# Performance work log

Measured on AMD Instinct MI355X. Metric: run time of the kernel, lower is better.

The kernel has to match this reference:

```python
import jax, jax.numpy as jnp
import numpy as np

B, N, DEG = 8, 4096, 16
E = N * DEG            # edges per graph
IN, HID, C, OUT = 128, 512, 2, 10
EPS = 1e-15


def setup_inputs() -> dict:
    key = jax.random.key(0)
    ks = jax.random.split(key, 16)
    # within-graph random edges, then offset each graph by b*N
    src = jax.random.randint(ks[0], (B, E), 0, N)
    dst = jax.random.randint(ks[1], (B, E), 0, N)
    off = (jnp.arange(B) * N)[:, None]
    edge_index = jnp.stack([(src + off).reshape(-1), (dst + off).reshape(-1)], axis=0).astype(jnp.int64)
    batch = jnp.repeat(jnp.arange(B), N).astype(jnp.int64)
    x = jax.random.normal(ks[2], (B * N, IN), dtype=jnp.float32)
    edge_weight = jax.random.uniform(ks[3], (B * E,), dtype=jnp.float32)
    g = lambda k, s: (0.02 * jax.random.normal(k, s, dtype=jnp.float32))
    return {
        "x": x, "edge_index": edge_index, "batch": batch, "edge_weight": edge_weight,
        "W_rel1": g(ks[4], (IN, HID)), "b_rel1": jnp.zeros((HID,), jnp.float32),
        "W_root1": g(ks[5], (IN, HID)),
        "W_pool": g(ks[6], (HID, C)), "b_pool": jnp.zeros((C,), jnp.float32),
        "W_rel3": g(ks[7], (HID, HID)), "b_rel3": jnp.zeros((HID,), jnp.float32),
        "W_root3": g(ks[8], (HID, HID)),
        "W_lin1": g(ks[9], (HID, HID)), "b_lin1": jnp.zeros((HID,), jnp.float32),
        "W_lin2": g(ks[10], (HID, OUT)), "b_lin2": jnp.zeros((OUT,), jnp.float32),
    }


def reference(x, edge_index, batch, edge_weight,
              W_rel1, b_rel1, W_root1, W_pool, b_pool,
              W_rel3, b_rel3, W_root3, W_lin1, b_lin1, W_lin2, b_lin2):
    src, dst = edge_index[0], edge_index[1]
    # GraphConv (aggr='add'): out = lin_rel(sum_j w_ji x_j) + lin_root(x)
    agg = jax.ops.segment_sum(x[src] * edge_weight[:, None], dst, num_segments=B * N)
    h = jax.nn.relu(agg @ W_rel1 + b_rel1 + x @ W_root1)          # [BN, HID]
    s_logits = h @ W_pool + b_pool                                 # [BN, C]

    # dense batched tensors (equal-size graphs)
    hd = h.reshape(B, N, HID)
    s = jax.nn.softmax(s_logits.reshape(B, N, C), axis=-1)
    b_idx = batch[src]
    r = src - b_idx * N
    c = dst - b_idx * N
    adj = jnp.zeros((B, N, N), jnp.float32).at[b_idx, r, c].add(edge_weight)

    # dense mincut pooling
    out = jnp.einsum('bnc,bnf->bcf', s, hd)                        # [B, C, HID]
    sA = jnp.einsum('bnc,bnm->bcm', s, adj)
    out_adj = jnp.einsum('bcm,bmk->bck', sA, s)                    # [B, C, C]
    mincut_num = jnp.einsum('bcc->b', out_adj)
    d = adj.sum(-1)                                                # [B, N]
    mincut_den = jnp.einsum('bnc,bn,bnc->b', s, d, s)
    mc_loss = jnp.mean(-(mincut_num / mincut_den))
    ss = jnp.einsum('bnc,bnk->bck', s, s)
    ss_n = ss / jnp.linalg.norm(ss, axis=(1, 2), keepdims=True)
    i_s = jnp.eye(C, dtype=jnp.float32) / jnp.sqrt(jnp.float32(C))
    o_loss = jnp.mean(jnp.linalg.norm(ss_n - i_s[None], axis=(1, 2)))
    # zero diagonal + symmetric degree normalization
    out_adj = out_adj * (1.0 - jnp.eye(C, dtype=jnp.float32))[None]
    d2 = jnp.sqrt(out_adj.sum(-1)) + EPS                           # [B, C]
    out_adj = out_adj / d2[:, :, None] / d2[:, None, :]

    # conv3 on pooled graph: edges (row->col) of dense adj => agg = A^T x
    agg3 = jnp.einsum('bij,bif->bjf', out_adj, out)
    x3 = agg3 @ W_rel3 + b_rel3 + out @ W_root3                    # [B, C, HID]
    xm = x3.mean(axis=1)                                           # [B, HID]
    h2 = jax.nn.relu(xm @ W_lin1 + b_lin1)
    logits = h2 @ W_lin2 + b_lin2
    return (jax.nn.log_softmax(logits, axis=-1), mc_loss, o_loss, s_logits, out_adj)
```

## Files before the change

### kernel.cpp

```cpp
#include <hip/hip_runtime.h>
#include <hip/hip_bf16.h>

#define BB 8
#define NN 4096
#define EE 65536
#define BE (BB*EE)
#define BN (BB*NN)
#define INF 128
#define HID 512
#define CC 2
#define OUTC 10
#define ELLCAP 64

typedef __bf16 bf16x8_t __attribute__((ext_vector_type(8)));
typedef float  f32x4_t  __attribute__((ext_vector_type(4)));

__device__ __forceinline__ ushort f2bf(float f) {
  union { float f; unsigned u; } v; v.f = f;
  unsigned r = v.u + 0x7FFFu + ((v.u >> 16) & 1u);
  return (ushort)(r >> 16);
}
__device__ __forceinline__ float bf2f(ushort s) {
  union { unsigned u; float f; } v; v.u = ((unsigned)s) << 16;
  return v.f;
}

__global__ __launch_bounds__(256) void front(
    const int* __restrict__ src, const int* __restrict__ dst,
    const float* __restrict__ ew, const float* __restrict__ x,
    const float* __restrict__ Wrel, const float* __restrict__ Wroot,
    int* __restrict__ deg, int2* __restrict__ ell,
    ushort* __restrict__ Ab, ushort* __restrict__ Bb) {
  int blk = blockIdx.x;
  int tid = threadIdx.x;
  if (blk < 4096) {
    int g = (blk & 7) * 131072 + (blk >> 3) * 256 + tid;
    float4 v = *(const float4*)&x[(size_t)g * 4];
    int m = g >> 5;
    int kin = (g & 31) * 4;
    ushort4 o;
    o.x = f2bf(v.x); o.y = f2bf(v.y); o.z = f2bf(v.z); o.w = f2bf(v.w);
    *(ushort4*)&Ab[(size_t)m * 256 + 128 + kin] = o;
  } else if (blk < 6144) {
    int bl = blk - 4096;
    int e = (bl & 7) * EE + (bl >> 3) * 256 + tid;
    int d = dst[e];
    int p = atomicAdd(&deg[d], 1);
    if (p < ELLCAP) {
      int2 v; v.x = src[e]; v.y = __float_as_int(ew[e]);
      ell[(size_t)d * ELLCAP + p] = v;
    }
  } else {
    int g = (blk - 6144) * 256 + tid;
    int n = g & 511, k = g >> 9;
    float w = (k < 128) ? Wrel[k * 512 + n] : Wroot[(k - 128) * 512 + n];
    Bb[n * 256 + k] = f2bf(w);
  }
}

__global__ __launch_bounds__(256) void gather_ell(
    const int* __restrict__ deg, const int2* __restrict__ ell,
    ushort* __restrict__ Ab) {
  int blk = blockIdx.x;
  int n = (blk & 7) * NN + (blk >> 3) * 4 + (threadIdx.x >> 6);
  int lane = threadIdx.x & 63;
  int l4 = lane >> 4;
  int fl = lane & 15;
  int d = deg[n]; if (d > ELLCAP) d = ELLCAP;
  const int2* ep = ell + (size_t)n * ELLCAP;

  float a[8] = {0, 0, 0, 0, 0, 0, 0, 0};
  int j = 0;
  for (; j + 7 < d; j += 8) {
    int2 v0 = ep[j + l4];
    int2 v1 = ep[j + 4 + l4];
    uint4 u0 = *(const uint4*)&Ab[(size_t)v0.x * 256 + 128 + fl * 8];
    uint4 u1 = *(const uint4*)&Ab[(size_t)v1.x * 256 + 128 + fl * 8];
    float w0 = __int_as_float(v0.y);
    float w1 = __int_as_float(v1.y);
    const ushort* s0 = (const ushort*)&u0;
    const ushort* s1 = (const ushort*)&u1;
#pragma unroll
    for (int q = 0; q < 8; ++q)
      a[q] += w0 * bf2f(s0[q]) + w1 * bf2f(s1[q]);
  }
  for (; j + 3 < d; j += 4) {
    int2 v0 = ep[j + l4];
    uint4 u0 = *(const uint4*)&Ab[(size_t)v0.x * 256 + 128 + fl * 8];
    float w0 = __int_as_float(v0.y);
    const ushort* s0 = (const ushort*)&u0;
#pragma unroll
    for (int q = 0; q < 8; ++q)
      a[q] += w0 * bf2f(s0[q]);
  }
  {
    int idx = j + l4;
    if (idx < d) {
      int2 v0 = ep[idx];
      uint4 u0 = *(const uint4*)&Ab[(size_t)v0.x * 256 + 128 + fl * 8];
      float w0 = __int_as_float(v0.y);
      const ushort* s0 = (const ushort*)&u0;
#pragma unroll
      for (int q = 0; q < 8; ++q)
        a[q] += w0 * bf2f(s0[q]);
    }
  }
#pragma unroll
  for (int q = 0; q < 8; ++q) {
    a[q] += __shfl_xor(a[q], 16, 64);
    a[q] += __shfl_xor(a[q], 32, 64);
  }
  if (l4 == 0) {
    ushort o[8];
#pragma unroll
    for (int q = 0; q < 8; ++q) o[q] = f2bf(a[q]);
    *(uint4*)&Ab[(size_t)n * 256 + fl * 8] = *(const uint4*)o;
  }
}

__global__ __launch_bounds__(256) void gemm_pool(
    const ushort* __restrict__ Ab, const ushort* __restrict__ Bb,
    const float* __restrict__ brel, const float* __restrict__ Wp,
    const float* __restrict__ bp, float* __restrict__ s,
    float* __restrict__ slog, float* __restrict__ outpart,
    float* __restrict__ ssacc) {
  __shared__ ushort As[64 * 256];
  __shared__ ushort Bs[64 * 256];
  __shared__ ushort hS[64 * 512];
  __shared__ float ssr[4][3];
  int tid = threadIdx.x;
  int blk = blockIdx.x;
  int b = blk & 7;
  int chunk = blk >> 3;
  int m0 = b * NN + chunk * 64;
  int obik = b * 64 + chunk;

#pragma unroll
  for (int i = 0; i < 8; ++i) {
    int g = tid + i * 256;
    int r = g >> 5, c = g & 31;
    int cs = c ^ (r & 31);
    *(uint4*)&As[(r * 32 + cs) * 8] = *(const uint4*)&Ab[(size_t)(m0 + r) * 256 + c * 8];
  }

  int wave = tid >> 6, lane = tid & 63;
  int wm = wave * 16;
  int l16 = lane & 15, quad = lane >> 4;
  int arow = wm + l16;

  for (int cc = 0; cc < 8; ++cc) {
    int n0 = cc * 64;
#pragma unroll
    for (int i = 0; i < 8; ++i) {
      int g = tid + i * 256;
      int r = g >> 5, c = g & 31;
      int cs = c ^ (r & 31);
      *(uint4*)&Bs[(r * 32 + cs) * 8] = *(const uint4*)&Bb[(size_t)(n0 + r) * 256 + c * 8];
    }
    __syncthreads();

    f32x4_t acc[4];
#pragma unroll
    for (int ct = 0; ct < 4; ++ct) acc[ct] = (f32x4_t){0.f, 0.f, 0.f, 0.f};
#pragma unroll
    for (int kc = 0; kc < 8; ++kc) {
      int cl = kc * 4 + quad;
      bf16x8_t af = *(const bf16x8_t*)&As[(arow * 32 + (cl ^ (arow & 31))) * 8];
#pragma unroll
      for (int ct = 0; ct < 4; ++ct) {
        int brow = ct * 16 + l16;
        bf16x8_t bf = *(const bf16x8_t*)&Bs[(brow * 32 + (cl ^ (brow & 31))) * 8];
        acc[ct] = __builtin_amdgcn_mfma_f32_16x16x32_bf16(af, bf, acc[ct], 0, 0, 0);
      }
    }
#pragma unroll
    for (int ct = 0; ct < 4; ++ct) {
      int col = n0 + ct * 16 + l16;
      float bias = brel[col];
      int rowb = wm + quad * 4;
#pragma unroll
      for (int r = 0; r < 4; ++r)
        hS[(rowb + r) * 512 + col] = f2bf(fmaxf(acc[ct][r] + bias, 0.f));
    }
    __syncthreads();
  }

  int f0 = lane * 8;
  float wp0[8], wp1[8];
#pragma unroll
  for (int j = 0; j < 8; ++j) {
    wp0[j] = Wp[(f0 + j) * 2];
    wp1[j] = Wp[(f0 + j) * 2 + 1];
  }
  float bp0 = bp[0], bp1 = bp[1];
  float o0[8] = {0, 0, 0, 0, 0, 0, 0, 0};
  float o1[8] = {0, 0, 0, 0, 0, 0, 0, 0};
  float sa = 0.f, sb = 0.f, sc2 = 0.f;

  for (int i = 0; i < 16; ++i) {
    int nl = wm + i;
    int n = m0 + nl;
    bf16x8_t hv = *(const bf16x8_t*)&hS[(size_t)nl * 512 + f0];
    const ushort* hp = (const ushort*)&hv;
    float h[8];
    float a0 = 0.f, a1 = 0.f;
#pragma unroll
    for (int j = 0; j < 8; ++j) {
      h[j] = bf2f(hp[j]);
      a0 += h[j] * wp0[j];
      a1 += h[j] * wp1[j];
    }
#pragma unroll
    for (int off = 32; off; off >>= 1) {
      a0 += __shfl_down(a0, off, 64);
      a1 += __shfl_down(a1, off, 64);
    }
    float s0 = 0.f, s1 = 0.f;
    if (lane == 0) {
      float l0 = a0 + bp0, l1 = a1 + bp1;
      slog[n * 2] = l0;
      slog[n * 2 + 1] = l1;
      float m = fmaxf(l0, l1);
      float e0 = expf(l0 - m), e1 = expf(l1 - m);
      float inv = 1.f / (e0 + e1);
      s0 = e0 * inv; s1 = e1 * inv;
      s[n * 2] = s0;
      s[n * 2 + 1] = s1;
      sa += s0 * s0; sb += s0 * s1; sc2 += s1 * s1;
    }
    s0 = __shfl(s0, 0, 64);
    s1 = __shfl(s1, 0, 64);
#pragma unroll
    for (int j = 0; j < 8; ++j) {
      o0[j] += s0 * h[j];
      o1[j] += s1 * h[j];
    }
  }

  float* red = (float*)As;
#pragma unroll
  for (int j = 0; j < 8; ++j) {
    red[wave * 1024 + f0 + j] = o0[j];
    red[wave * 1024 + 512 + f0 + j] = o1[j];
  }
  if (lane == 0) { ssr[wave][0] = sa; ssr[wave][1] = sb; ssr[wave][2] = sc2; }
  __syncthreads();
#pragma unroll
  for (int q = 0; q < 4; ++q) {
    int idx = tid + q * 256;
    float v = red[idx] + red[1024 + idx] + red[2048 + idx] + red[3072 + idx];
    outpart[(size_t)obik * 1024 + idx] = v;
  }
  if (tid < 3) {
    float v = ssr[0][tid] + ssr[1][tid] + ssr[2][tid] + ssr[3][tid];
    atomicAdd(&ssacc[b * 4 + tid], v);
  }
}

__global__ __launch_bounds__(256) void edge_pass2(
    const int* __restrict__ src, const int* __restrict__ dst,
    const float* __restrict__ ew, const float* __restrict__ s,
    float* __restrict__ oadj, float* __restrict__ mden) {
  int b = blockIdx.x & 7;
  int sub = blockIdx.x >> 3;
  int base = b * EE + sub * 1024;
  float p00 = 0, p01 = 0, p10 = 0, p11 = 0, md = 0;
  for (int i = threadIdx.x; i < 1024; i += 256) {
    int e = base + i;
    int r = src[e], c = dst[e];
    float w = ew[e];
    float s0r = s[r * 2], s1r = s[r * 2 + 1];
    float s0c = s[c * 2], s1c = s[c * 2 + 1];
    p00 += w * s0r * s0c; p01 += w * s0r * s1c;
    p10 += w * s1r * s0c; p11 += w * s1r * s1c;
    md  += w * (s0r * s0r + s1r * s1r);
  }
#pragma unroll
  for (int off = 32; off; off >>= 1) {
    p00 += __shfl_down(p00, off, 64);
    p01 += __shfl_down(p01, off, 64);
    p10 += __shfl_down(p10, off, 64);
    p11 += __shfl_down(p11, off, 64);
    md  += __shfl_down(md,  off, 64);
  }
  __shared__ float red[4][5];
  int wave = threadIdx.x >> 6, lane = threadIdx.x & 63;
  if (lane == 0) {
    red[wave][0] = p00; red[wave][1] = p01;
    red[wave][2] = p10; red[wave][3] = p11;
    red[wave][4] = md;
  }
  __syncthreads();
  if (threadIdx.x < 4) {
    float v = red[0][threadIdx.x] + red[1][threadIdx.x] +
              red[2][threadIdx.x] + red[3][threadIdx.x];
    atomicAdd(&oadj[b * 4 + threadIdx.x], v);
  } else if (threadIdx.x == 4) {
    float v = red[0][4] + red[1][4] + red[2][4] + red[3][4];
    atomicAdd(&mden[b], v);
  }
}

__global__ __launch_bounds__(256) void finalize_a(
    const float* __restrict__ outpart, const float* __restrict__ oadj,
    const float* __restrict__ ssacc, const float* __restrict__ mden,
    float* __restrict__ uv, float* __restrict__ lossp,
    float* __restrict__ dout) {
  __shared__ float sc[2];
  __shared__ float r0[256], r1[256];
  int b = blockIdx.x >> 3, fc = blockIdx.x & 7;
  int t = threadIdx.x;
  if (t == 0) {
    float r00 = oadj[b * 4 + 0], r01 = oadj[b * 4 + 1];
    float r10 = oadj[b * 4 + 2], r11 = oadj[b * 4 + 3];
    float d20 = sqrtf(r01) + 1e-15f;
    float d21 = sqrtf(r10) + 1e-15f;
    float oa01 = r01 / (d20 * d21);
    float oa10 = r10 / (d21 * d20);
    sc[0] = oa01; sc[1] = oa10;
    if (fc == 0) {
      lossp[b * 2 + 0] = -((r00 + r11) / mden[b]) / (float)BB;
      float a = ssacc[b * 4 + 0], bb = ssacc[b * 4 + 1], c = ssacc[b * 4 + 2];
      float nrm = sqrtf(a * a + 2.f * bb * bb + c * c);
      float q = 0.70710678118654752f;
      float da = a / nrm - q, db = bb / nrm, dc = c / nrm - q;
      lossp[b * 2 + 1] = sqrtf(da * da + 2.f * db * db + dc * dc) / (float)BB;
      dout[65618 + b * 4 + 0] = 0.f;
      dout[65618 + b * 4 + 1] = oa01;
      dout[65618 + b * 4 + 2] = oa10;
      dout[65618 + b * 4 + 3] = 0.f;
    }
  }
  __syncthreads();
  int f = fc * 64 + (t & 63);
  int ic = t >> 6;
  float o0s = 0.f, o1s = 0.f;
  for (int i = ic * 16; i < ic * 16 + 16; ++i) {
    o0s += outpart[(size_t)(b * 64 + i) * 1024 + f];
    o1s += outpart[(size_t)(b * 64 + i) * 1024 + 512 + f];
  }
  r0[ic * 64 + (t & 63)] = o0s;
  r1[ic * 64 + (t & 63)] = o1s;
  __syncthreads();
  if (ic == 0) {
    int fl = t & 63;
    float a0 = r0[fl] + r0[64 + fl] + r0[128 + fl] + r0[192 + fl];
    float a1 = r1[fl] + r1[64 + fl] + r1[128 + fl] + r1[192 + fl];
    uv[b * HID + f] = sc[1] * a1 + sc[0] * a0;
    uv[BB * HID + b * HID + f] = a0 + a1;
  }
}

__global__ __launch_bounds__(256) void conv3_part(
    const float* __restrict__ uv, const float* __restrict__ Wrel3,
    const float* __restrict__ Wroot3, float* __restrict__ xmacc) {
  __shared__ float us[8][32], vs[8][32];
  __shared__ float red[4][64][8];
  int blk = blockIdx.x;
  int fc = blk & 7, kc = blk >> 3;
  int t = threadIdx.x;
  {
    int b = t >> 5, k = t & 31;
    us[b][k] = uv[b * HID + kc * 32 + k];
    vs[b][k] = uv[BB * HID + b * HID + kc * 32 + k];
  }
  __syncthreads();
  int f = fc * 64 + (t & 63);
  int ks = t >> 6;
  float acc[8] = {0, 0, 0, 0, 0, 0, 0, 0};
#pragma unroll
  for (int j = 0; j < 8; ++j) {
    int kl = ks * 8 + j;
    int k = kc * 32 + kl;
    float wr = Wrel3[k * HID + f];
    float wo = Wroot3[k * HID + f];
#pragma unroll
    for (int b = 0; b < 8; ++b)
      acc[b] += us[b][kl] * wr + vs[b][kl] * wo;
  }
#pragma unroll
  for (int b = 0; b < 8; ++b) red[ks][t & 63][b] = acc[b];
  __syncthreads();
  if (ks == 0) {
    int fl = t & 63;
#pragma unroll
    for (int b = 0; b < 8; ++b) {
      float v = red[0][fl][b] + red[1][fl][b] + red[2][fl][b] + red[3][fl][b];
      atomicAdd(&xmacc[b * HID + f], v);
    }
  }
}

__global__ __launch_bounds__(256) void lin1_part(
    const float* __restrict__ xmacc, const float* __restrict__ brel3,
    const float* __restrict__ Wlin1, float* __restrict__ h2acc) {
  __shared__ float xs[8][32];
  __shared__ float red[4][64][8];
  int blk = blockIdx.x;
  int fc = blk & 7, kc = blk >> 3;
  int t = threadIdx.x;
  {
    int b = t >> 5, k = t & 31;
    xs[b][k] = 0.5f * xmacc[b * HID + kc * 32 + k] + brel3[kc * 32 + k];
  }
  __syncthreads();
  int f = fc * 64 + (t & 63);
  int ks = t >> 6;
  float acc[8] = {0, 0, 0, 0, 0, 0, 0, 0};
#pragma unroll
  for (int j = 0; j < 8; ++j) {
    int kl = ks * 8 + j;
    int k = kc * 32 + kl;
    float w = Wlin1[k * HID + f];
#pragma unroll
    for (int b = 0; b < 8; ++b)
      acc[b] += xs[b][kl] * w;
  }
#pragma unroll
  for (int b = 0; b < 8; ++b) red[ks][t & 63][b] = acc[b];
  __syncthreads();
  if (ks == 0) {
    int fl = t & 63;
#pragma unroll
    for (int b = 0; b < 8; ++b) {
      float v = red[0][fl][b] + red[1][fl][b] + red[2][fl][b] + red[3][fl][b];
      atomicAdd(&h2acc[b * HID + f], v);
    }
  }
}

__global__ __launch_bounds__(256) void head(
    const float* __restrict__ h2acc, const float* __restrict__ blin1,
    const float* __restrict__ Wlin2, const float* __restrict__ blin2,
    const float* __restrict__ lossp, float* __restrict__ dout) {
  __shared__ float hs[HID];
  __shared__ float lg[16];
  __shared__ float lse;
  int b = blockIdx.x, t = threadIdx.x;
  if (b == 0 && t == 255) {
    float l0 = 0.f, l1 = 0.f;
#pragma unroll
    for (int i = 0; i < BB; ++i) { l0 += lossp[i * 2]; l1 += lossp[i * 2 + 1]; }
    dout[80] = l0;
    dout[81] = l1;
  }
  for (int i = t; i < HID; i += 256)
    hs[i] = fmaxf(h2acc[b * HID + i] + blin1[i], 0.f);
  __syncthreads();
  int wave = t >> 6, lane = t & 63;
  for (int o = wave; o < OUTC; o += 4) {
    float acc = 0.f;
    for (int k = lane; k < HID; k += 64)
      acc += hs[k] * Wlin2[k * OUTC + o];
#pragma unroll
    for (int off = 32; off; off >>= 1) acc += __shfl_down(acc, off, 64);
    if (lane == 0) lg[o] = acc + blin2[o];
  }
  __syncthreads();
  if (t == 0) {
    float m = lg[0];
    for (int o = 1; o < OUTC; ++o) m = fmaxf(m, lg[o]);
    float se = 0.f;
    for (int o = 0; o < OUTC; ++o) se += expf(lg[o] - m);
    lse = m + logf(se);
  }
  __syncthreads();
  if (t < OUTC) dout[b * OUTC + t] = lg[t] - lse;
}

extern "C" void kernel_launch(void* const* d_in, const int* in_sizes, int n_in,
                              void* d_out, int out_size, void* d_ws, size_t ws_size,
                              hipStream_t stream) {
  const float* x      = (const float*)d_in[0];
  const int*   ei     = (const int*)d_in[1];
  const float* ew     = (const float*)d_in[3];
  const float* Wrel1  = (const float*)d_in[4];
  const float* brel1  = (const float*)d_in[5];
  const float* Wroot1 = (const float*)d_in[6];
  const float* Wpool  = (const float*)d_in[7];
  const float* bpool  = (const float*)d_in[8];
  const float* Wrel3  = (const float*)d_in[9];
  const float* brel3  = (const float*)d_in[10];
  const float* Wroot3 = (const float*)d_in[11];
  const float* Wlin1  = (const float*)d_in[12];
  const float* blin1  = (const float*)d_in[13];
  const float* Wlin2  = (const float*)d_in[14];
  const float* blin2  = (const float*)d_in[15];
  float* out = (float*)d_out;
  float* ws  = (float*)d_ws;

  float* oadj  = ws + 40960;
  float* ssacc = oadj + 32;
  float* mden  = ssacc + 32;
  int*   deg   = (int*)(mden + 8);
  float* xmacc = ws + 73800;
  float* h2acc = xmacc + 4096;
  float* lossp = ws + 81992;
  ushort* Ab   = (ushort*)(ws + 106568);
  ushort* Bb   = (ushort*)(ws + 4300872);
  float* outpart = ws + 12763208;
  float* s     = ws + 16000000;
  int2*  ell   = (int2*)(ws + 4366408);
  float* uv    = (float*)deg;

  const int* src = ei;
  const int* dst = ei + BE;

  hipMemsetAsync(ws + 40960, 0, (size_t)41032 * sizeof(float), stream);

  front      <<<6656, 256, 0, stream>>>(src, dst, ew, x, Wrel1, Wroot1,
                                        deg, ell, Ab, Bb);
  gather_ell <<<BN / 4, 256, 0, stream>>>(deg, ell, Ab);
  gemm_pool  <<<512, 256, 0, stream>>>(Ab, Bb, brel1, Wpool, bpool,
                                       s, out + 82, outpart, ssacc);
  edge_pass2 <<<BB * 64, 256, 0, stream>>>(src, dst, ew, s, oadj, mden);
  finalize_a <<<64, 256, 0, stream>>>(outpart, oadj, ssacc, mden, uv, lossp, out);
  conv3_part <<<128, 256, 0, stream>>>(uv, Wrel3, Wroot3, xmacc);
  lin1_part  <<<128, 256, 0, stream>>>(xmacc, brel3, Wlin1, h2acc);
  head       <<<BB, 256, 0, stream>>>(h2acc, blin1, Wlin2, blin2, lossp, out);
}
```

Baseline: 209.7 us.

## Recompute conv1 GEMM in gemm_pool instead of staging h in LDS

Drops the 64 KB LDS buffer that held the bf16 hidden tile. The pool logits are now accumulated straight from the MFMA outputs, and the whole GEMM is run a second time to build the softmax-weighted feature sums, which are reduced into a small LDS array with atomics. This cuts LDS use per block so more blocks can be resident. In exchange it doubles the MFMA work and the B-matrix loads.

```diff
diff --git a/kernel.cpp b/kernel.cpp
--- a/kernel.cpp
+++ b/kernel.cpp
@@ -126,8 +126,11 @@
     float* __restrict__ ssacc) {
   __shared__ ushort As[64 * 256];
   __shared__ ushort Bs[64 * 256];
-  __shared__ ushort hS[64 * 512];
-  __shared__ float ssr[4][3];
+  __shared__ float wpS[1024];
+  __shared__ float brS[512];
+  __shared__ float2 ssv[64];
+  __shared__ float ssrw[16][3];
+  __shared__ float oacc[1024];
   int tid = threadIdx.x;
   int blk = blockIdx.x;
   int b = blk & 7;
@@ -142,11 +145,17 @@
     int cs = c ^ (r & 31);
     *(uint4*)&As[(r * 32 + cs) * 8] = *(const uint4*)&Ab[(size_t)(m0 + r) * 256 + c * 8];
   }
+  *(float4*)&wpS[tid * 4] = *(const float4*)&Wp[tid * 4];
+  if (tid < 128) *(float4*)&brS[tid * 4] = *(const float4*)&brel[tid * 4];
+  *(float4*)&oacc[tid * 4] = (float4){0.f, 0.f, 0.f, 0.f};
 
   int wave = tid >> 6, lane = tid & 63;
   int wm = wave * 16;
   int l16 = lane & 15, quad = lane >> 4;
   int arow = wm + l16;
+  float bp0 = bp[0], bp1 = bp[1];
+
+  float la0[4] = {0, 0, 0, 0}, la1[4] = {0, 0, 0, 0};
 
   for (int cc = 0; cc < 8; ++cc) {
     int n0 = cc * 64;
@@ -176,83 +185,105 @@
 #pragma unroll
     for (int ct = 0; ct < 4; ++ct) {
       int col = n0 + ct * 16 + l16;
-      float bias = brel[col];
-      int rowb = wm + quad * 4;
-#pragma unroll
-      for (int r = 0; r < 4; ++r)
-        hS[(rowb + r) * 512 + col] = f2bf(fmaxf(acc[ct][r] + bias, 0.f));
+      float bias = brS[col];
+      float w0 = wpS[col * 2], w1 = wpS[col * 2 + 1];
+#pragma unroll
+      for (int r = 0; r < 4; ++r) {
+        float h = fmaxf(acc[ct][r] + bias, 0.f);
+        la0[r] += h * w0;
+        la1[r] += h * w1;
+      }
     }
     __syncthreads();
   }
 
-  int f0 = lane * 8;
-  float wp0[8], wp1[8];
-#pragma unroll
-  for (int j = 0; j < 8; ++j) {
-    wp0[j] = Wp[(f0 + j) * 2];
-    wp1[j] = Wp[(f0 + j) * 2 + 1];
-  }
-  float bp0 = bp[0], bp1 = bp[1];
-  float o0[8] = {0, 0, 0, 0, 0, 0, 0, 0};
-  float o1[8] = {0, 0, 0, 0, 0, 0, 0, 0};
-  float sa = 0.f, sb = 0.f, sc2 = 0.f;
-
-  for (int i = 0; i < 16; ++i) {
-    int nl = wm + i;
-    int n = m0 + nl;
-    bf16x8_t hv = *(const bf16x8_t*)&hS[(size_t)nl * 512 + f0];
-    const ushort* hp = (const ushort*)&hv;
-    float h[8];
-    float a0 = 0.f, a1 = 0.f;
-#pragma unroll
-    for (int j = 0; j < 8; ++j) {
-      h[j] = bf2f(hp[j]);
-      a0 += h[j] * wp0[j];
-      a1 += h[j] * wp1[j];
-    }
-#pragma unroll
-    for (int off = 32; off; off >>= 1) {
-      a0 += __shfl_down(a0, off, 64);
-      a1 += __shfl_down(a1, off, 64);
-    }
-    float s0 = 0.f, s1 = 0.f;
-    if (lane == 0) {
-      float l0 = a0 + bp0, l1 = a1 + bp1;
+#pragma unroll
+  for (int r = 0; r < 4; ++r) {
+#pragma unroll
+    for (int m = 1; m < 16; m <<= 1) {
+      la0[r] += __shfl_xor(la0[r], m, 64);
+      la1[r] += __shfl_xor(la1[r], m, 64);
+    }
+  }
+  if (l16 == 0) {
+    float sa = 0.f, sb = 0.f, sc2 = 0.f;
+#pragma unroll
+    for (int r = 0; r < 4; ++r) {
+      int row = wm + quad * 4 + r;
+      int n = m0 + row;
+      float l0 = la0[r] + bp0, l1 = la1[r] + bp1;
       slog[n * 2] = l0;
       slog[n * 2 + 1] = l1;
-      float m = fmaxf(l0, l1);
-      float e0 = expf(l0 - m), e1 = expf(l1 - m);
+      float mm = fmaxf(l0, l1);
+      float e0 = expf(l0 - mm), e1 = expf(l1 - mm);
       float inv = 1.f / (e0 + e1);
-      s0 = e0 * inv; s1 = e1 * inv;
-      s[n * 2] = s0;
-      s[n * 2 + 1] = s1;
+      float s0 = e0 * inv, s1 = e1 * inv;
+      *(float2*)&s[n * 2] = make_float2(s0, s1);
+      ssv[row] = make_float2(s0, s1);
       sa += s0 * s0; sb += s0 * s1; sc2 += s1 * s1;
     }
-    s0 = __shfl(s0, 0, 64);
-    s1 = __shfl(s1, 0, 64);
-#pragma unroll
-    for (int j = 0; j < 8; ++j) {
-      o0[j] += s0 * h[j];
-      o1[j] += s1 * h[j];
-    }
-  }
-
-  float* red = (float*)As;
-#pragma unroll
-  for (int j = 0; j < 8; ++j) {
-    red[wave * 1024 + f0 + j] = o0[j];
-    red[wave * 1024 + 512 + f0 + j] = o1[j];
-  }
-  if (lane == 0) { ssr[wave][0] = sa; ssr[wave][1] = sb; ssr[wave][2] = sc2; }
-  __syncthreads();
+    int idx = wave * 4 + quad;
+    ssrw[idx][0] = sa; ssrw[idx][1] = sb; ssrw[idx][2] = sc2;
+  }
+  __syncthreads();
+
+  for (int cc = 0; cc < 8; ++cc) {
+    int n0 = cc * 64;
+#pragma unroll
+    for (int i = 0; i < 8; ++i) {
+      int g = tid + i * 256;
+      int r = g >> 5, c = g & 31;
+      int cs = c ^ (r & 31);
+      *(uint4*)&Bs[(r * 32 + cs) * 8] = *(const uint4*)&Bb[(size_t)(n0 + r) * 256 + c * 8];
+    }
+    __syncthreads();
+
+    f32x4_t acc[4];
+#pragma unroll
+    for (int ct = 0; ct < 4; ++ct) acc[ct] = (f32x4_t){0.f, 0.f, 0.f, 0.f};
+#pragma unroll
+    for (int kc = 0; kc < 8; ++kc) {
+      int cl = kc * 4 + quad;
+      bf16x8_t af = *(const bf16x8_t*)&As[(arow * 32 + (cl ^ (arow & 31))) * 8];
+#pragma unroll
+      for (int ct = 0; ct < 4; ++ct) {
+        int brow = ct * 16 + l16;
+        bf16x8_t bf = *(const bf16x8_t*)&Bs[(brow * 32 + (cl ^ (brow & 31))) * 8];
+        acc[ct] = __builtin_amdgcn_mfma_f32_16x16x32_bf16(af, bf, acc[ct], 0, 0, 0);
+      }
+    }
+#pragma unroll
+    for (int ct = 0; ct < 4; ++ct) {
+      int col = n0 + ct * 16 + l16;
+      float bias = brS[col];
+      float v0 = 0.f, v1 = 0.f;
+#pragma unroll
+      for (int r = 0; r < 4; ++r) {
+        int row = wm + quad * 4 + r;
+        float2 sv = ssv[row];
+        float h = fmaxf(acc[ct][r] + bias, 0.f);
+        v0 += sv.x * h;
+        v1 += sv.y * h;
+      }
+      v0 += __shfl_xor(v0, 16, 64); v0 += __shfl_xor(v0, 32, 64);
+      v1 += __shfl_xor(v1, 16, 64); v1 += __shfl_xor(v1, 32, 64);
+      if (lane < 16) {
+        atomicAdd(&oacc[col], v0);
+        atomicAdd(&oacc[512 + col], v1);
+      }
+    }
+    __syncthreads();
+  }
+
 #pragma unroll
   for (int q = 0; q < 4; ++q) {
     int idx = tid + q * 256;
-    float v = red[idx] + red[1024 + idx] + red[2048 + idx] + red[3072 + idx];
-    outpart[(size_t)obik * 1024 + idx] = v;
+    outpart[(size_t)obik * 1024 + idx] = oacc[idx];
   }
   if (tid < 3) {
-    float v = ssr[0][tid] + ssr[1][tid] + ssr[2][tid] + ssr[3][tid];
+    float v = 0.f;
+#pragma unroll
+    for (int i = 0; i < 16; ++i) v += ssrw[i][tid];
     atomicAdd(&ssacc[b * 4 + tid], v);
   }
 }
```

Result: no change. 208.0 us (-0.8%).
